# Performance work log

Hardware: AMD Instinct MI355X
Metric: run time of the kernel (lower is better)

## Reference

```python
import jax, jax.numpy as jnp
import numpy as np

B, S, D, H, E, TOPK = 4, 2048, 1024, 1024, 8, 2

def setup_inputs() -> dict:
    key = jax.random.key(0)
    k1, k2, k3 = jax.random.split(key, 3)
    x = jax.random.normal(k1, (B, S, D), dtype=jnp.float32)
    Wg = jax.random.normal(k2, (D, E), dtype=jnp.float32) * (1.0 / np.sqrt(D))
    bg = jnp.zeros((E,), dtype=jnp.float32)
    We = jax.random.normal(k3, (E, D, H), dtype=jnp.float32) * (1.0 / np.sqrt(D))
    be = jnp.zeros((E, H), dtype=jnp.float32)
    return {"x": x, "Wg": Wg, "bg": bg, "We": We, "be": be, "k": TOPK}

def reference(x, Wg, bg, We, be, k):
    # gate logits: [B, S, E]
    logits = jnp.einsum('bsd,de->bse', x, Wg) + bg
    # top-k gating (values, indices along expert axis)
    top_vals, sel = jax.lax.top_k(logits, k)            # [B, S, k]
    weights = jax.nn.softmax(top_vals.astype(jnp.float32), axis=-1).astype(x.dtype)
    # per-token combine weight for each expert: [B, S, E]
    onehot = jax.nn.one_hot(sel, E, dtype=x.dtype)      # [B, S, k, E]
    comb = jnp.einsum('bsk,bske->bse', weights, onehot)
    # all-expert dense outputs (equivalent math to per-expert gather+GEMM+scatter)
    y = jnp.einsum('bsd,edh->besh', x, We) + be[None, :, None, :]  # [B, E, S, H]
    out = jnp.einsum('bse,besh->bsh', comb, y)          # [B, S, H]
    return out
```

## Files before the change

### kernel.cpp

```cpp
#include <hip/hip_runtime.h>
#include <hip/hip_bf16.h>
#include <hip/hip_fp16.h>

#define NTOK 8192
#define DDIM 1024
#define HDIM 1024
#define NEXP 8

typedef __attribute__((ext_vector_type(8))) short short8;
typedef __attribute__((ext_vector_type(4))) float f32x4;
typedef __attribute__((ext_vector_type(4))) unsigned short us4;
typedef __attribute__((ext_vector_type(8))) unsigned short us8;

static __device__ __forceinline__ unsigned short f2bf(float f) {
  union { float f; unsigned u; } v; v.f = f;
  return (unsigned short)((v.u + 0x7fffu + ((v.u >> 16) & 1u)) >> 16);
}

static __device__ __forceinline__ void gload16(const void* g, void* l) {
  __builtin_amdgcn_global_load_lds(
      (const __attribute__((address_space(1))) unsigned int*)g,
      (__attribute__((address_space(3))) unsigned int*)l, 16, 0, 0);
}

__global__ __launch_bounds__(256) void wg_transpose(
    const float* __restrict__ Wg, float* __restrict__ wgT)
{
  const int i = blockIdx.x * 256 + threadIdx.x;
  const int e = i >> 10, d = i & 1023;
  wgT[i] = Wg[d * NEXP + e];
}

__global__ __launch_bounds__(256) void gate_kernel(
    const float* __restrict__ x, const float* __restrict__ wgT,
    const float* __restrict__ bg, unsigned short* __restrict__ xb,
    int* __restrict__ sel, float* __restrict__ wts)
{
  __shared__ float wg[NEXP * DDIM];
  const int tid = threadIdx.x;
#pragma unroll
  for (int i = 0; i < 8; ++i) {
    const int o = (i * 256 + tid) * 4;
    *(float4*)&wg[o] = *(const float4*)&wgT[o];
  }
  __syncthreads();

  const int wave = tid >> 6;
  const int lane = tid & 63;

  for (int t = 0; t < 4; ++t) {
    const int token = blockIdx.x * 16 + wave * 4 + t;
    const float* xr = x + (size_t)token * DDIM;

    float acc[NEXP];
#pragma unroll
    for (int e = 0; e < NEXP; ++e) acc[e] = 0.f;

#pragma unroll
    for (int q = 0; q < 4; ++q) {
      const int d0 = q * 256 + lane * 4;
      const float4 xv = *(const float4*)(xr + d0);
      us4 hb;
      hb.x = f2bf(xv.x); hb.y = f2bf(xv.y); hb.z = f2bf(xv.z); hb.w = f2bf(xv.w);
      *(us4*)(xb + (size_t)token * DDIM + d0) = hb;
#pragma unroll
      for (int e = 0; e < NEXP; ++e) {
        const float4 wv = *(const float4*)&wg[e * DDIM + d0];
        acc[e] += xv.x * wv.x;
        acc[e] += xv.y * wv.y;
        acc[e] += xv.z * wv.z;
        acc[e] += xv.w * wv.w;
      }
    }

#pragma unroll
    for (int e = 0; e < NEXP; ++e) {
#pragma unroll
      for (int off = 32; off >= 1; off >>= 1)
        acc[e] += __shfl_xor(acc[e], off, 64);
    }

    if (lane == 0) {
      float v[NEXP];
#pragma unroll
      for (int e = 0; e < NEXP; ++e) v[e] = acc[e] + bg[e];
      int i0 = 0; float v0 = v[0];
#pragma unroll
      for (int e = 1; e < NEXP; ++e) if (v[e] > v0) { v0 = v[e]; i0 = e; }
      int i1 = -1; float v1 = -3.4e38f;
#pragma unroll
      for (int e = 0; e < NEXP; ++e) if (e != i0 && v[e] > v1) { v1 = v[e]; i1 = e; }
      const float tt = __expf(v1 - v0);
      const float w0 = 1.f / (1.f + tt);
      const float w1 = tt / (1.f + tt);
      sel[token * 2 + 0] = i0;  wts[token * 2 + 0] = w0;
      sel[token * 2 + 1] = i1;  wts[token * 2 + 1] = w1;
    }
  }
}

__global__ __launch_bounds__(256) void route_kernel(
    const int* __restrict__ sel, const float* __restrict__ wts,
    int* __restrict__ counts, int* __restrict__ tlist, float* __restrict__ wlist,
    int* __restrict__ dstrow)
{
  __shared__ int bin[NEXP];
  __shared__ int base[NEXP];
  const int tid = threadIdx.x;
  if (tid < NEXP) bin[tid] = 0;
  __syncthreads();
  const int idx = blockIdx.x * 256 + tid;
  const int e = sel[idx];
  const float w = wts[idx];
  const int rank = atomicAdd(&bin[e], 1);
  __syncthreads();
  if (tid < NEXP) base[tid] = atomicAdd(&counts[tid], bin[tid]);
  __syncthreads();
  const int pos = base[e] + rank;
  tlist[e * NTOK + pos] = idx >> 1;
  wlist[e * NTOK + pos] = w;
  dstrow[e * NTOK + pos] = idx;
}

__global__ __launch_bounds__(256) void transpose_we(
    const float* __restrict__ We, unsigned short* __restrict__ wbt)
{
  const int e = blockIdx.z;
  const int h0 = blockIdx.x * 64;
  const int d0 = blockIdx.y * 128;
  __shared__ float t[128][65];
  const int tx = threadIdx.x;

  {
    const int hc = (tx & 15) * 4;
    const float* src = We + ((size_t)e * DDIM + d0) * HDIM + h0 + hc;
#pragma unroll
    for (int i = 0; i < 8; ++i) {
      const int dr = (tx >> 4) + i * 16;
      const float4 v = *(const float4*)(src + (size_t)dr * HDIM);
      t[dr][hc] = v.x; t[dr][hc + 1] = v.y; t[dr][hc + 2] = v.z; t[dr][hc + 3] = v.w;
    }
  }
  __syncthreads();
  {
    const int dc = (tx & 7) * 16;
#pragma unroll
    for (int i2 = 0; i2 < 2; ++i2) {
      const int hr = (tx >> 3) + i2 * 32;
      us8 o0, o1;
#pragma unroll
      for (int j = 0; j < 8; ++j) ((unsigned short*)&o0)[j] = f2bf(t[dc + j][hr]);
#pragma unroll
      for (int j = 0; j < 8; ++j) ((unsigned short*)&o1)[j] = f2bf(t[dc + 8 + j][hr]);
      unsigned short* dst = wbt + ((size_t)e * HDIM + h0 + hr) * DDIM + d0 + dc;
      *(us8*)dst = o0;
      *(us8*)(dst + 8) = o1;
    }
  }
}

__global__ __launch_bounds__(512, 4) void moe_gemm(
    const unsigned short* __restrict__ xb,
    const unsigned short* __restrict__ wbt,
    const float* __restrict__ be,
    const int* __restrict__ counts,
    const int* __restrict__ tlist,
    const float* __restrict__ wlist,
    const int* __restrict__ dstrow,
    __half* __restrict__ yb)
{
  const int e = blockIdx.z;
  const int cnt = counts[e];
  const int tile = blockIdx.y;
  if (tile * 256 >= cnt) return;
  const int n0 = blockIdx.x * 128;

  __shared__ unsigned short As[256 * 64];
  __shared__ unsigned short Bs[128 * 64];

  const int tid = threadIdx.x;
  const int lane = tid & 63;
  const int wv = tid >> 6;
  const int wm = wv >> 1;
  const int wn = wv & 1;

  const int rA = tid >> 3;
  const int kbA = (tid & 7) << 4;
  const unsigned short* aSrc[4];
  const unsigned short* bSrc[2];
  int ldsA[4]; int ldsB[2];
#pragma unroll
  for (int q = 0; q < 4; ++q) {
    const int r = q * 64 + rA;
    int trow = tile * 256 + r;
    trow = trow < cnt ? trow : cnt - 1;
    const int tok = tlist[e * NTOK + trow];
    const int kbs = kbA ^ ((r & 7) << 4);
    aSrc[q] = xb + (size_t)tok * DDIM + (kbs >> 1);
    ldsA[q] = r * 64 + (kbA >> 1);
  }
#pragma unroll
  for (int q = 0; q < 2; ++q) {
    const int r = q * 64 + rA;
    const int kbs = kbA ^ ((r & 7) << 4);
    bSrc[q] = wbt + ((size_t)e * HDIM + n0 + r) * DDIM + (kbs >> 1);
    ldsB[q] = r * 64 + (kbA >> 1);
  }

  f32x4 acc[4][4];
#pragma unroll
  for (int m = 0; m < 4; ++m)
#pragma unroll
    for (int n = 0; n < 4; ++n)
      acc[m][n] = (f32x4){0.f, 0.f, 0.f, 0.f};

  for (int kt = 0; kt < DDIM / 64; ++kt) {
    __syncthreads();
#pragma unroll
    for (int q = 0; q < 4; ++q) gload16(aSrc[q] + kt * 64, &As[ldsA[q]]);
#pragma unroll
    for (int q = 0; q < 2; ++q) gload16(bSrc[q] + kt * 64, &Bs[ldsB[q]]);
    __syncthreads();

#pragma unroll
    for (int kk = 0; kk < 2; ++kk) {
      const int kb = kk * 64 + ((lane >> 4) << 4);
      short8 af[4], bfr[4];
#pragma unroll
      for (int m = 0; m < 4; ++m) {
        const int r = wm * 64 + m * 16 + (lane & 15);
        af[m] = *(const short8*)((const char*)As + r * 128 + (kb ^ ((r & 7) << 4)));
      }
#pragma unroll
      for (int n = 0; n < 4; ++n) {
        const int r = wn * 64 + n * 16 + (lane & 15);
        bfr[n] = *(const short8*)((const char*)Bs + r * 128 + (kb ^ ((r & 7) << 4)));
      }
#pragma unroll
      for (int m = 0; m < 4; ++m)
#pragma unroll
        for (int n = 0; n < 4; ++n)
          acc[m][n] = __builtin_amdgcn_mfma_f32_16x16x32_bf16(af[m], bfr[n], acc[m][n], 0, 0, 0);
    }
  }

  const int rbase = wm * 64 + ((lane >> 4) << 2);
  const int cb = lane & 15;
  float bev[4];
#pragma unroll
  for (int n = 0; n < 4; ++n) bev[n] = be[e * HDIM + n0 + wn * 64 + n * 16 + cb];
#pragma unroll
  for (int m = 0; m < 4; ++m) {
#pragma unroll
    for (int r4 = 0; r4 < 4; ++r4) {
      const int trow = tile * 256 + rbase + m * 16 + r4;
      if (trow < cnt) {
        const int drow = dstrow[e * NTOK + trow];
        const float w = wlist[e * NTOK + trow];
        __half* yrow = yb + (size_t)drow * HDIM + n0 + wn * 64 + cb;
#pragma unroll
        for (int n = 0; n < 4; ++n)
          yrow[n * 16] = __float2half(w * (acc[m][n][r4] + bev[n]));
      }
    }
  }
}

__global__ __launch_bounds__(256) void combine_kernel(
    const __half* __restrict__ yb, float* __restrict__ out)
{
  const int g = blockIdx.x * 256 + threadIdx.x;
  const int tok = g >> 7;
  const int h0 = (g & 127) * 8;
  const short8 p0 = *(const short8*)(yb + ((size_t)tok * 2) * HDIM + h0);
  const short8 p1 = *(const short8*)(yb + ((size_t)tok * 2 + 1) * HDIM + h0);
  float r[8];
#pragma unroll
  for (int j = 0; j < 8; ++j) {
    __half a = *(const __half*)&((const short*)&p0)[j];
    __half b = *(const __half*)&((const short*)&p1)[j];
    r[j] = __half2float(a) + __half2float(b);
  }
  float* o = out + (size_t)tok * HDIM + h0;
  *(float4*)o = (float4){r[0], r[1], r[2], r[3]};
  *(float4*)(o + 4) = (float4){r[4], r[5], r[6], r[7]};
}

extern "C" void kernel_launch(void* const* d_in, const int* in_sizes, int n_in,
                              void* d_out, int out_size, void* d_ws, size_t ws_size,
                              hipStream_t stream)
{
  const float* x  = (const float*)d_in[0];
  const float* Wg = (const float*)d_in[1];
  const float* bg = (const float*)d_in[2];
  const float* We = (const float*)d_in[3];
  const float* be = (const float*)d_in[4];

  char* ws = (char*)d_ws;
  int*   counts = (int*)ws;
  int*   tlist  = (int*)(ws + 256);
  float* wlist  = (float*)(ws + 256 + NEXP * NTOK * 4);
  int*   dstrow = (int*)(ws + 256 + 2 * NEXP * NTOK * 4);
  int*   sel    = (int*)(ws + 256 + 3 * NEXP * NTOK * 4);
  float* wts    = (float*)(ws + 256 + 3 * NEXP * NTOK * 4 + 2 * NTOK * 4);
  float* wgT    = (float*)(ws + 0x180000);
  unsigned short* xb  = (unsigned short*)(ws + (1 << 21));
  unsigned short* wbt = (unsigned short*)(ws + (1 << 21) + (size_t)NTOK * DDIM * 2);
  __half* yb = (__half*)(ws + (1 << 21) + 2 * (size_t)NTOK * DDIM * 2);
  float* out = (float*)d_out;

  hipMemsetAsync(counts, 0, 256, stream);

  wg_transpose<<<32, 256, 0, stream>>>(Wg, wgT);
  gate_kernel<<<NTOK / 16, 256, 0, stream>>>(x, wgT, bg, xb, sel, wts);
  route_kernel<<<2 * NTOK / 256, 256, 0, stream>>>(sel, wts, counts, tlist, wlist, dstrow);
  transpose_we<<<dim3(HDIM / 64, DDIM / 128, NEXP), 256, 0, stream>>>(We, wbt);
  moe_gemm<<<dim3(HDIM / 128, NTOK / 256, NEXP), 512, 0, stream>>>(
      xb, wbt, be, counts, tlist, wlist, dstrow, yb);
  combine_kernel<<<NTOK * HDIM / 8 / 256, 256, 0, stream>>>(yb, out);
}
```

Before: 201.5 us.

## Fuse gate, Wg transpose and We transpose into one prep kernel

Merges the Wg transpose, gating/bf16 conversion, We transpose and the counts memset into a single prep kernel whose blocks are split by role, so the gating and weight conversion run concurrently instead of as separate launches. The gate now transposes Wg into shared memory directly. The MoE GEMM is also split into two launches over halves of the experts. This removes several launches and the memset, but the split GEMM adds a launch and may leave the GPU underfilled at the boundary. Counts are zeroed by one block with no ordering guarantee against other blocks, which is safe only because the route kernel runs after prep finishes.

```diff
diff --git a/kernel.cpp b/kernel.cpp
--- a/kernel.cpp
+++ b/kernel.cpp
@@ -23,78 +23,117 @@
       (__attribute__((address_space(3))) unsigned int*)l, 16, 0, 0);
 }
 
-__global__ __launch_bounds__(256) void wg_transpose(
-    const float* __restrict__ Wg, float* __restrict__ wgT)
-{
-  const int i = blockIdx.x * 256 + threadIdx.x;
-  const int e = i >> 10, d = i & 1023;
-  wgT[i] = Wg[d * NEXP + e];
-}
-
-__global__ __launch_bounds__(256) void gate_kernel(
-    const float* __restrict__ x, const float* __restrict__ wgT,
+__global__ __launch_bounds__(256) void prep_kernel(
+    const float* __restrict__ x, const float* __restrict__ Wg,
     const float* __restrict__ bg, unsigned short* __restrict__ xb,
-    int* __restrict__ sel, float* __restrict__ wts)
-{
-  __shared__ float wg[NEXP * DDIM];
+    int* __restrict__ sel, float* __restrict__ wts,
+    const float* __restrict__ We, unsigned short* __restrict__ wbt,
+    int* __restrict__ counts)
+{
+  __shared__ float smem[128 * 65];
+  const int bi = blockIdx.x;
   const int tid = threadIdx.x;
-#pragma unroll
-  for (int i = 0; i < 8; ++i) {
-    const int o = (i * 256 + tid) * 4;
-    *(float4*)&wg[o] = *(const float4*)&wgT[o];
-  }
-  __syncthreads();
-
-  const int wave = tid >> 6;
-  const int lane = tid & 63;
-
-  for (int t = 0; t < 4; ++t) {
-    const int token = blockIdx.x * 16 + wave * 4 + t;
-    const float* xr = x + (size_t)token * DDIM;
-
-    float acc[NEXP];
-#pragma unroll
-    for (int e = 0; e < NEXP; ++e) acc[e] = 0.f;
-
-#pragma unroll
-    for (int q = 0; q < 4; ++q) {
-      const int d0 = q * 256 + lane * 4;
-      const float4 xv = *(const float4*)(xr + d0);
-      us4 hb;
-      hb.x = f2bf(xv.x); hb.y = f2bf(xv.y); hb.z = f2bf(xv.z); hb.w = f2bf(xv.w);
-      *(us4*)(xb + (size_t)token * DDIM + d0) = hb;
+
+  if (bi < NTOK / 16) {
+    float* wg = smem;
+#pragma unroll
+    for (int k = 0; k < 4; ++k) {
+      const int d = tid + k * 256;
+      const float4 a = *(const float4*)(Wg + d * NEXP);
+      const float4 b = *(const float4*)(Wg + d * NEXP + 4);
+      wg[0 * DDIM + d] = a.x; wg[1 * DDIM + d] = a.y;
+      wg[2 * DDIM + d] = a.z; wg[3 * DDIM + d] = a.w;
+      wg[4 * DDIM + d] = b.x; wg[5 * DDIM + d] = b.y;
+      wg[6 * DDIM + d] = b.z; wg[7 * DDIM + d] = b.w;
+    }
+    __syncthreads();
+
+    const int wave = tid >> 6;
+    const int lane = tid & 63;
+
+    for (int t = 0; t < 4; ++t) {
+      const int token = bi * 16 + wave * 4 + t;
+      const float* xr = x + (size_t)token * DDIM;
+
+      float acc[NEXP];
+#pragma unroll
+      for (int e = 0; e < NEXP; ++e) acc[e] = 0.f;
+
+#pragma unroll
+      for (int q = 0; q < 4; ++q) {
+        const int d0 = q * 256 + lane * 4;
+        const float4 xv = *(const float4*)(xr + d0);
+        us4 hb;
+        hb.x = f2bf(xv.x); hb.y = f2bf(xv.y); hb.z = f2bf(xv.z); hb.w = f2bf(xv.w);
+        *(us4*)(xb + (size_t)token * DDIM + d0) = hb;
+#pragma unroll
+        for (int e = 0; e < NEXP; ++e) {
+          const float4 wv = *(const float4*)&wg[e * DDIM + d0];
+          acc[e] += xv.x * wv.x;
+          acc[e] += xv.y * wv.y;
+          acc[e] += xv.z * wv.z;
+          acc[e] += xv.w * wv.w;
+        }
+      }
+
 #pragma unroll
       for (int e = 0; e < NEXP; ++e) {
-        const float4 wv = *(const float4*)&wg[e * DDIM + d0];
-        acc[e] += xv.x * wv.x;
-        acc[e] += xv.y * wv.y;
-        acc[e] += xv.z * wv.z;
-        acc[e] += xv.w * wv.w;
-      }
-    }
-
-#pragma unroll
-    for (int e = 0; e < NEXP; ++e) {
-#pragma unroll
-      for (int off = 32; off >= 1; off >>= 1)
-        acc[e] += __shfl_xor(acc[e], off, 64);
-    }
-
-    if (lane == 0) {
-      float v[NEXP];
-#pragma unroll
-      for (int e = 0; e < NEXP; ++e) v[e] = acc[e] + bg[e];
-      int i0 = 0; float v0 = v[0];
-#pragma unroll
-      for (int e = 1; e < NEXP; ++e) if (v[e] > v0) { v0 = v[e]; i0 = e; }
-      int i1 = -1; float v1 = -3.4e38f;
-#pragma unroll
-      for (int e = 0; e < NEXP; ++e) if (e != i0 && v[e] > v1) { v1 = v[e]; i1 = e; }
-      const float tt = __expf(v1 - v0);
-      const float w0 = 1.f / (1.f + tt);
-      const float w1 = tt / (1.f + tt);
-      sel[token * 2 + 0] = i0;  wts[token * 2 + 0] = w0;
-      sel[token * 2 + 1] = i1;  wts[token * 2 + 1] = w1;
+#pragma unroll
+        for (int off = 32; off >= 1; off >>= 1)
+          acc[e] += __shfl_xor(acc[e], off, 64);
+      }
+
+      if (lane == 0) {
+        float v[NEXP];
+#pragma unroll
+        for (int e = 0; e < NEXP; ++e) v[e] = acc[e] + bg[e];
+        int i0 = 0; float v0 = v[0];
+#pragma unroll
+        for (int e = 1; e < NEXP; ++e) if (v[e] > v0) { v0 = v[e]; i0 = e; }
+        int i1 = -1; float v1 = -3.4e38f;
+#pragma unroll
+        for (int e = 0; e < NEXP; ++e) if (e != i0 && v[e] > v1) { v1 = v[e]; i1 = e; }
+        const float tt = __expf(v1 - v0);
+        const float w0 = 1.f / (1.f + tt);
+        const float w1 = tt / (1.f + tt);
+        sel[token * 2 + 0] = i0;  wts[token * 2 + 0] = w0;
+        sel[token * 2 + 1] = i1;  wts[token * 2 + 1] = w1;
+      }
+    }
+  } else {
+    const int b = bi - NTOK / 16;
+    if (b == 0 && tid < 64) counts[tid] = 0;
+    const int e = b >> 7;
+    const int rem = b & 127;
+    const int h0 = (rem & 15) * 64;
+    const int d0 = (rem >> 4) * 128;
+    float (*t)[65] = (float(*)[65])smem;
+
+    {
+      const int hc = (tid & 15) * 4;
+      const float* src = We + ((size_t)e * DDIM + d0) * HDIM + h0 + hc;
+#pragma unroll
+      for (int i = 0; i < 8; ++i) {
+        const int dr = (tid >> 4) + i * 16;
+        const float4 v = *(const float4*)(src + (size_t)dr * HDIM);
+        t[dr][hc] = v.x; t[dr][hc + 1] = v.y; t[dr][hc + 2] = v.z; t[dr][hc + 3] = v.w;
+      }
+    }
+    __syncthreads();
+    {
+      const int dc = (tid & 7) * 16;
+#pragma unroll
+      for (int i2 = 0; i2 < 2; ++i2) {
+        const int hr = (tid >> 3) + i2 * 32;
+        us8 o0, o1;
+#pragma unroll
+        for (int j = 0; j < 8; ++j) ((unsigned short*)&o0)[j] = f2bf(t[dc + j][hr]);
+#pragma unroll
+        for (int j = 0; j < 8; ++j) ((unsigned short*)&o1)[j] = f2bf(t[dc + 8 + j][hr]);
+        unsigned short* dst = wbt + ((size_t)e * HDIM + h0 + hr) * DDIM + d0 + dc;
+        *(us8*)dst = o0;
+        *(us8*)(dst + 8) = o1;
+      }
     }
   }
 }
@@ -122,43 +161,6 @@
   dstrow[e * NTOK + pos] = idx;
 }
 
-__global__ __launch_bounds__(256) void transpose_we(
-    const float* __restrict__ We, unsigned short* __restrict__ wbt)
-{
-  const int e = blockIdx.z;
-  const int h0 = blockIdx.x * 64;
-  const int d0 = blockIdx.y * 128;
-  __shared__ float t[128][65];
-  const int tx = threadIdx.x;
-
-  {
-    const int hc = (tx & 15) * 4;
-    const float* src = We + ((size_t)e * DDIM + d0) * HDIM + h0 + hc;
-#pragma unroll
-    for (int i = 0; i < 8; ++i) {
-      const int dr = (tx >> 4) + i * 16;
-      const float4 v = *(const float4*)(src + (size_t)dr * HDIM);
-      t[dr][hc] = v.x; t[dr][hc + 1] = v.y; t[dr][hc + 2] = v.z; t[dr][hc + 3] = v.w;
-    }
-  }
-  __syncthreads();
-  {
-    const int dc = (tx & 7) * 16;
-#pragma unroll
-    for (int i2 = 0; i2 < 2; ++i2) {
-      const int hr = (tx >> 3) + i2 * 32;
-      us8 o0, o1;
-#pragma unroll
-      for (int j = 0; j < 8; ++j) ((unsigned short*)&o0)[j] = f2bf(t[dc + j][hr]);
-#pragma unroll
-      for (int j = 0; j < 8; ++j) ((unsigned short*)&o1)[j] = f2bf(t[dc + 8 + j][hr]);
-      unsigned short* dst = wbt + ((size_t)e * HDIM + h0 + hr) * DDIM + d0 + dc;
-      *(us8*)dst = o0;
-      *(us8*)(dst + 8) = o1;
-    }
-  }
-}
-
 __global__ __launch_bounds__(512, 4) void moe_gemm(
     const unsigned short* __restrict__ xb,
     const unsigned short* __restrict__ wbt,
@@ -167,9 +169,9 @@
     const int* __restrict__ tlist,
     const float* __restrict__ wlist,
     const int* __restrict__ dstrow,
-    __half* __restrict__ yb)
-{
-  const int e = blockIdx.z;
+    __half* __restrict__ yb, const int ebase)
+{
+  const int e = blockIdx.z + ebase;
   const int cnt = counts[e];
   const int tile = blockIdx.y;
   if (tile * 256 >= cnt) return;
@@ -303,19 +305,17 @@
   int*   dstrow = (int*)(ws + 256 + 2 * NEXP * NTOK * 4);
   int*   sel    = (int*)(ws + 256 + 3 * NEXP * NTOK * 4);
   float* wts    = (float*)(ws + 256 + 3 * NEXP * NTOK * 4 + 2 * NTOK * 4);
-  float* wgT    = (float*)(ws + 0x180000);
   unsigned short* xb  = (unsigned short*)(ws + (1 << 21));
   unsigned short* wbt = (unsigned short*)(ws + (1 << 21) + (size_t)NTOK * DDIM * 2);
   __half* yb = (__half*)(ws + (1 << 21) + 2 * (size_t)NTOK * DDIM * 2);
   float* out = (float*)d_out;
 
-  hipMemsetAsync(counts, 0, 256, stream);
-
-  wg_transpose<<<32, 256, 0, stream>>>(Wg, wgT);
-  gate_kernel<<<NTOK / 16, 256, 0, stream>>>(x, wgT, bg, xb, sel, wts);
+  prep_kernel<<<NTOK / 16 + NEXP * 128, 256, 0, stream>>>(
+      x, Wg, bg, xb, sel, wts, We, wbt, counts);
   route_kernel<<<2 * NTOK / 256, 256, 0, stream>>>(sel, wts, counts, tlist, wlist, dstrow);
-  transpose_we<<<dim3(HDIM / 64, DDIM / 128, NEXP), 256, 0, stream>>>(We, wbt);
-  moe_gemm<<<dim3(HDIM / 128, NTOK / 256, NEXP), 512, 0, stream>>>(
-      xb, wbt, be, counts, tlist, wlist, dstrow, yb);
+  moe_gemm<<<dim3(HDIM / 128, NTOK / 256, NEXP / 2), 512, 0, stream>>>(
+      xb, wbt, be, counts, tlist, wlist, dstrow, yb, 0);
+  moe_gemm<<<dim3(HDIM / 128, NTOK / 256, NEXP / 2), 512, 0, stream>>>(
+      xb, wbt, be, counts, tlist, wlist, dstrow, yb, NEXP / 2);
   combine_kernel<<<NTOK * HDIM / 8 / 256, 256, 0, stream>>>(yb, out);
 }
```

After: 198.7 us. No clear change (-1.4%).
